# Optimization experiments

Hardware: AMD Instinct MI355X
Metric: run time of the kernel (lower is better)

Reference implementation:

```python
import jax, jax.numpy as jnp
import numpy as np

SIGMA = 5.67e-8  # Stefan-Boltzmann constant
NX = 13
N = NX * NX  # 169 nodes
B = 131072


def _build_matrices(L=0.1, thickness=0.001, board_k=15.0, emis=0.8):
    dx = L / (NX - 1)
    dy = L / (NX - 1)
    GLx = thickness * board_k * dy / dx
    GLy = thickness * board_k * dx / dy
    GR = 2.0 * dx * dy * emis
    iface = {0, NX - 1, NX * NX - 1, NX * NX - NX}
    K = np.zeros((N, N), dtype=np.float32)
    for j in range(NX):
        for i in range(NX):
            idn = i + NX * j
            if idn in iface:
                K[idn, idn] = 1.0
            else:
                gii = 0.0
                if i + 1 < NX:
                    K[idn, idn + 1] = -GLx  # east
                    gii += GLx
                if i - 1 >= 0:
                    K[idn, idn - 1] = -GLx  # west
                    gii += GLx
                if j + 1 < NX:
                    K[idn, idn + NX] = -GLx  # north (original code uses -GLx here too)
                    gii += GLy
                if j - 1 >= 0:
                    K[idn, idn - NX] = -GLx  # south (original code uses -GLx here too)
                    gii += GLy
                K[idn, idn] = gii
    e = np.full(N, GR, dtype=np.float32)
    for t in iface:
        e[t] = 0.0
    return jnp.asarray(K), jnp.asarray(e)


def setup_inputs() -> dict:
    key = jax.random.key(0)
    k1, k2, k3, k4 = jax.random.split(key, 4)
    # realistic temperatures (K) and heat loads (W)
    outputs = 270.0 + 60.0 * jax.random.uniform(k1, (B, NX, NX), dtype=jnp.float32)
    heaters = 0.5 * jax.random.uniform(k2, (B, NX, NX), dtype=jnp.float32)
    interfaces = 0.5 * jax.random.uniform(k3, (B, NX, NX), dtype=jnp.float32)
    Tenv = 270.0 + 30.0 * jax.random.uniform(k4, (B, 1), dtype=jnp.float32)
    K, e_diag = _build_matrices()
    return {"outputs": outputs, "heaters": heaters, "interfaces": interfaces,
            "Tenv": Tenv, "K": K, "e_diag": e_diag}


def reference(outputs, heaters, interfaces, Tenv, K, e_diag):
    b = outputs.shape[0]
    T = outputs.reshape(b, -1)                    # [B, 169]
    Q = heaters.reshape(b, -1) + interfaces.reshape(b, -1)  # [B, 169]
    # original computes K @ T_nodes_x_batch; batch-major equivalent is T @ K^T
    conduction = jnp.einsum('bn,mn->bm', T, K)    # [B, 169]
    radiation = SIGMA * e_diag[None, :] * (T ** 4 - Tenv ** 4)  # Tenv [B,1] broadcasts
    excess = conduction + radiation - Q
    return jnp.mean(jnp.abs(excess))
```

## Files before the change

### kernel.cpp

```cpp
#include <hip/hip_runtime.h>
#include <math.h>


#define SIGMA_F 5.67e-8f

constexpr int BLOCK = 256;

typedef float f4a __attribute__((ext_vector_type(4), aligned(4)));
typedef float f4b __attribute__((ext_vector_type(4), aligned(16)));

__global__ __launch_bounds__(256) void fused_residual_v7(
    const float* __restrict__ T,
    const float* __restrict__ H,
    const float* __restrict__ F,
    const float* __restrict__ Tenv,
    const float* __restrict__ K,
    const float* __restrict__ Ediag,
    float* __restrict__ partials,
    int total)
{
    __shared__ unsigned sTab[176];
    __shared__ float sred[BLOCK / 64];

    const float GLx = -K[1 * 169 + 2];
    const float GRs = SIGMA_F * Ediag[1];

    const int tid  = (int)threadIdx.x;
    const int lane = tid & 63;

    if (tid < 176) {
        int m = (tid < 169) ? tid : tid - 169;
        int ii = m % 13;
        unsigned cW = (ii > 0)   ? 1u : 0u;
        unsigned cE = (ii < 12)  ? 1u : 0u;
        unsigned cN = (m < 156)  ? 1u : 0u;
        unsigned cS = (m >= 13)  ? 1u : 0u;
        sTab[tid] = cW | (cE << 8) | (cN << 16) | (cS << 24);
    }
    __syncthreads();

    float acc = 0.0f;

    const int gstride = gridDim.x * BLOCK;
    for (int g = blockIdx.x * BLOCK + tid; g * 8 < total; g += gstride) {
        const int e0 = g * 8;
        const int waveBase = e0 - lane * 8;
        const bool fast = (waveBase >= 16) && (waveBase + 64 * 8 + 16 <= total);

        if (fast) {
            f4b t0 = *(const f4b*)(T + e0);
            f4b t1 = *(const f4b*)(T + e0 + 4);
            f4b h0 = __builtin_nontemporal_load((const f4b*)(H + e0));
            f4b h1 = __builtin_nontemporal_load((const f4b*)(H + e0 + 4));
            f4b f0 = __builtin_nontemporal_load((const f4b*)(F + e0));
            f4b f1 = __builtin_nontemporal_load((const f4b*)(F + e0 + 4));

            float sv[8];
            sv[0] = __shfl_up(t0.w, 2);
            sv[1] = __shfl_up(t1.x, 2);
            sv[2] = __shfl_up(t1.y, 2);
            sv[3] = __shfl_up(t1.z, 2);
            sv[4] = __shfl_up(t1.w, 2);
            sv[5] = __shfl_up(t0.x, 1);
            sv[6] = __shfl_up(t0.y, 1);
            sv[7] = __shfl_up(t0.z, 1);
            if (lane < 2) {
                f4a a = *(const f4a*)(T + e0 - 13);
                f4a b = *(const f4a*)(T + e0 - 9);
                sv[0] = a.x; sv[1] = a.y; sv[2] = a.z; sv[3] = a.w;
                sv[4] = b.x; sv[5] = b.y; sv[6] = b.z; sv[7] = b.w;
            }
            float nv[8];
            nv[0] = __shfl_down(t1.y, 1);
            nv[1] = __shfl_down(t1.z, 1);
            nv[2] = __shfl_down(t1.w, 1);
            nv[3] = __shfl_down(t0.x, 2);
            nv[4] = __shfl_down(t0.y, 2);
            nv[5] = __shfl_down(t0.z, 2);
            nv[6] = __shfl_down(t0.w, 2);
            nv[7] = __shfl_down(t1.x, 2);
            if (lane >= 62) {
                f4a a = *(const f4a*)(T + e0 + 13);
                f4a b = *(const f4a*)(T + e0 + 17);
                nv[0] = a.x; nv[1] = a.y; nv[2] = a.z; nv[3] = a.w;
                nv[4] = b.x; nv[5] = b.y; nv[6] = b.z; nv[7] = b.w;
            }
            float left = __shfl_up(t1.w, 1);
            if (lane == 0) left = T[e0 - 1];
            float right = __shfl_down(t0.x, 1);
            if (lane == 63) right = T[e0 + 8];

            const unsigned ue = (unsigned)e0;
            const unsigned b0 = ue / 169u;
            const int m0 = (int)(ue - b0 * 169u);

            float tvA = Tenv[b0];
            float tvB = tvA;
            if (m0 >= 162) tvB = Tenv[b0 + 1];
            const float tv4A = (tvA * tvA) * (tvA * tvA);
            const float tv4B = (tvB * tvB) * (tvB * tvB);

            const float tCv[8] = {t0.x, t0.y, t0.z, t0.w, t1.x, t1.y, t1.z, t1.w};
            const float tWv[8] = {left, t0.x, t0.y, t0.z, t0.w, t1.x, t1.y, t1.z};
            const float tEv[8] = {t0.y, t0.z, t0.w, t1.x, t1.y, t1.z, t1.w, right};
            const float hq[8]  = {h0.x + f0.x, h0.y + f0.y, h0.z + f0.z, h0.w + f0.w,
                                  h1.x + f1.x, h1.y + f1.y, h1.z + f1.z, h1.w + f1.w};

            #pragma unroll
            for (int j = 0; j < 8; ++j) {
                const unsigned w = sTab[m0 + j];
                const float mW = (float)(w & 0xffu);
                const float mE = (float)((w >> 8) & 0xffu);
                const float mN = (float)((w >> 16) & 0xffu);
                const float mS = (float)(w >> 24);

                const float t = tCv[j];
                float s = mW * tWv[j];
                s = fmaf(mE, tEv[j], s);
                s = fmaf(mN, nv[j], s);
                s = fmaf(mS, sv[j], s);
                const float nn = (mW + mE) + (mN + mS);
                const float q  = hq[j];
                const float tv4 = (m0 + j >= 169) ? tv4B : tv4A;
                const float t2 = t * t;
                const float d  = fmaf(t2, t2, -tv4);
                const float core = fmaf(GLx, fmaf(nn, t, -s), fmaf(GRs, d, -q));
                const float ex = (nn == 2.0f) ? (t - q) : core;
                acc += fabsf(ex);
            }
        } else {
            #pragma unroll
            for (int j = 0; j < 8; ++j) {
                int e = e0 + j;
                if (e >= total) break;
                unsigned b = (unsigned)e / 169u;
                int m = e - (int)b * 169;
                unsigned q13 = (unsigned)m / 13u;
                int ii = m - (int)q13 * 13;
                bool cE = (ii < 12), cW = (ii > 0), cN = (m < 156), cS = (m >= 13);
                bool ifc = (m == 0) | (m == 12) | (m == 156) | (m == 168);
                float t  = T[e];
                float tEv2 = cE ? T[e + 1]  : 0.0f;
                float tWv2 = cW ? T[e - 1]  : 0.0f;
                float tNv2 = cN ? T[e + 13] : 0.0f;
                float tSv2 = cS ? T[e - 13] : 0.0f;
                float s  = tEv2 + tWv2 + tNv2 + tSv2;
                float nn = (float)((int)cE + (int)cW + (int)cN + (int)cS);
                float tv = Tenv[b];
                float tv4 = (tv * tv) * (tv * tv);
                float t2 = t * t, t4 = t2 * t2;
                float qq = H[e] + F[e];
                float ex = ifc ? (t - qq)
                               : (GLx * (nn * t - s) + GRs * (t4 - tv4) - qq);
                acc += fabsf(ex);
            }
        }
    }

    #pragma unroll
    for (int off = 32; off > 0; off >>= 1)
        acc += __shfl_down(acc, off, 64);
    const int wid = tid >> 6;
    if (lane == 0) sred[wid] = acc;
    __syncthreads();
    if (tid == 0) {
        float s = 0.0f;
        #pragma unroll
        for (int w = 0; w < BLOCK / 64; ++w) s += sred[w];
        partials[blockIdx.x] = s;
    }
}

__global__ __launch_bounds__(256) void finalize_kernel(
    const float* __restrict__ partials, int n,
    float* __restrict__ out, float inv_total)
{
    __shared__ float sred[BLOCK / 64];
    float acc = 0.0f;
    for (int i = (int)threadIdx.x; i < n; i += BLOCK) acc += partials[i];
    #pragma unroll
    for (int off = 32; off > 0; off >>= 1)
        acc += __shfl_down(acc, off, 64);
    int lane = threadIdx.x & 63;
    int wid  = threadIdx.x >> 6;
    if (lane == 0) sred[wid] = acc;
    __syncthreads();
    if (threadIdx.x == 0) {
        float s = 0.0f;
        #pragma unroll
        for (int w = 0; w < BLOCK / 64; ++w) s += sred[w];
        out[0] = s * inv_total;
    }
}

extern "C" void kernel_launch(void* const* d_in, const int* in_sizes, int n_in,
                              void* d_out, int out_size, void* d_ws, size_t ws_size,
                              hipStream_t stream) {
    const float* T    = (const float*)d_in[0];
    const float* H    = (const float*)d_in[1];
    const float* F    = (const float*)d_in[2];
    const float* Tenv = (const float*)d_in[3];
    const float* K    = (const float*)d_in[4];
    const float* E    = (const float*)d_in[5];
    float* out      = (float*)d_out;
    float* partials = (float*)d_ws;

    const int total = in_sizes[0];

    int grid = (total / 8 + BLOCK - 1) / BLOCK;
    if ((size_t)grid * sizeof(float) > ws_size) grid = (int)(ws_size / sizeof(float));
    if (grid < 1) grid = 1;

    fused_residual_v7<<<grid, BLOCK, 0, stream>>>(T, H, F, Tenv, K, E, partials, total);

    const float inv_total = 1.0f / (float)total;
    finalize_kernel<<<1, BLOCK, 0, stream>>>(partials, grid, out, inv_total);
}
```

Before: 244.8 us.

## Software-pipeline loads in a persistent grid-stride loop with capped grid

Switches from one block per work tile to a fixed grid of 2048 blocks that loop grid-stride. Each iteration prefetches the next tile's T/H/F vectors into registers before computing the current one, with a sched_barrier to keep the loads issued early. The aim is to hide memory latency and cut block launch overhead. In exchange it raises register pressure, which may lower occupancy, and the sTab table grows to 184 entries.

Measured after the change: 243.2 us. About the same (-0.7%).

```diff
diff --git a/kernel.cpp b/kernel.cpp
--- a/kernel.cpp
+++ b/kernel.cpp
@@ -9,7 +9,7 @@
 typedef float f4a __attribute__((ext_vector_type(4), aligned(4)));
 typedef float f4b __attribute__((ext_vector_type(4), aligned(16)));
 
-__global__ __launch_bounds__(256) void fused_residual_v7(
+__global__ __launch_bounds__(256) void fused_residual_v10(
     const float* __restrict__ T,
     const float* __restrict__ H,
     const float* __restrict__ F,
@@ -19,7 +19,7 @@
     float* __restrict__ partials,
     int total)
 {
-    __shared__ unsigned sTab[176];
+    __shared__ unsigned sTab[184];
     __shared__ float sred[BLOCK / 64];
 
     const float GLx = -K[1 * 169 + 2];
@@ -28,13 +28,13 @@
     const int tid  = (int)threadIdx.x;
     const int lane = tid & 63;
 
-    if (tid < 176) {
+    if (tid < 184) {
         int m = (tid < 169) ? tid : tid - 169;
         int ii = m % 13;
-        unsigned cW = (ii > 0)   ? 1u : 0u;
-        unsigned cE = (ii < 12)  ? 1u : 0u;
-        unsigned cN = (m < 156)  ? 1u : 0u;
-        unsigned cS = (m >= 13)  ? 1u : 0u;
+        unsigned cW = (ii > 0)  ? 1u : 0u;
+        unsigned cE = (ii < 12) ? 1u : 0u;
+        unsigned cN = (m < 156) ? 1u : 0u;
+        unsigned cS = (m >= 13) ? 1u : 0u;
         sTab[tid] = cW | (cE << 8) | (cN << 16) | (cS << 24);
     }
     __syncthreads();
@@ -42,28 +42,56 @@
     float acc = 0.0f;
 
     const int gstride = gridDim.x * BLOCK;
-    for (int g = blockIdx.x * BLOCK + tid; g * 8 < total; g += gstride) {
+
+    auto isfast = [&](int gg) -> bool {
+        const int wb = gg * 8 - lane * 8;
+        return (wb >= 16) && (wb + 64 * 8 + 16 <= total);
+    };
+
+    int  g        = (int)blockIdx.x * BLOCK + tid;
+    bool haveCur  = (g * 8 < total);
+    bool fastCur  = haveCur && isfast(g);
+
+    f4b ct0, ct1, ch0, ch1, cf0, cf1;
+    if (fastCur) {
         const int e0 = g * 8;
-        const int waveBase = e0 - lane * 8;
-        const bool fast = (waveBase >= 16) && (waveBase + 64 * 8 + 16 <= total);
-
-        if (fast) {
-            f4b t0 = *(const f4b*)(T + e0);
-            f4b t1 = *(const f4b*)(T + e0 + 4);
-            f4b h0 = __builtin_nontemporal_load((const f4b*)(H + e0));
-            f4b h1 = __builtin_nontemporal_load((const f4b*)(H + e0 + 4));
-            f4b f0 = __builtin_nontemporal_load((const f4b*)(F + e0));
-            f4b f1 = __builtin_nontemporal_load((const f4b*)(F + e0 + 4));
+        ct0 = *(const f4b*)(T + e0);
+        ct1 = *(const f4b*)(T + e0 + 4);
+        ch0 = __builtin_nontemporal_load((const f4b*)(H + e0));
+        ch1 = __builtin_nontemporal_load((const f4b*)(H + e0 + 4));
+        cf0 = __builtin_nontemporal_load((const f4b*)(F + e0));
+        cf1 = __builtin_nontemporal_load((const f4b*)(F + e0 + 4));
+    }
+
+    while (haveCur) {
+        const int  gn    = g + gstride;
+        const bool haveN = (gn * 8 < total);
+        const bool fastN = haveN && isfast(gn);
+
+        f4b pt0, pt1, ph0, ph1, pf0, pf1;
+        if (fastN) {
+            const int en = gn * 8;
+            pt0 = *(const f4b*)(T + en);
+            pt1 = *(const f4b*)(T + en + 4);
+            ph0 = __builtin_nontemporal_load((const f4b*)(H + en));
+            ph1 = __builtin_nontemporal_load((const f4b*)(H + en + 4));
+            pf0 = __builtin_nontemporal_load((const f4b*)(F + en));
+            pf1 = __builtin_nontemporal_load((const f4b*)(F + en + 4));
+        }
+        __builtin_amdgcn_sched_barrier(0);
+
+        if (fastCur) {
+            const int e0 = g * 8;
 
             float sv[8];
-            sv[0] = __shfl_up(t0.w, 2);
-            sv[1] = __shfl_up(t1.x, 2);
-            sv[2] = __shfl_up(t1.y, 2);
-            sv[3] = __shfl_up(t1.z, 2);
-            sv[4] = __shfl_up(t1.w, 2);
-            sv[5] = __shfl_up(t0.x, 1);
-            sv[6] = __shfl_up(t0.y, 1);
-            sv[7] = __shfl_up(t0.z, 1);
+            sv[0] = __shfl_up(ct0.w, 2);
+            sv[1] = __shfl_up(ct1.x, 2);
+            sv[2] = __shfl_up(ct1.y, 2);
+            sv[3] = __shfl_up(ct1.z, 2);
+            sv[4] = __shfl_up(ct1.w, 2);
+            sv[5] = __shfl_up(ct0.x, 1);
+            sv[6] = __shfl_up(ct0.y, 1);
+            sv[7] = __shfl_up(ct0.z, 1);
             if (lane < 2) {
                 f4a a = *(const f4a*)(T + e0 - 13);
                 f4a b = *(const f4a*)(T + e0 - 9);
@@ -71,23 +99,23 @@
                 sv[4] = b.x; sv[5] = b.y; sv[6] = b.z; sv[7] = b.w;
             }
             float nv[8];
-            nv[0] = __shfl_down(t1.y, 1);
-            nv[1] = __shfl_down(t1.z, 1);
-            nv[2] = __shfl_down(t1.w, 1);
-            nv[3] = __shfl_down(t0.x, 2);
-            nv[4] = __shfl_down(t0.y, 2);
-            nv[5] = __shfl_down(t0.z, 2);
-            nv[6] = __shfl_down(t0.w, 2);
-            nv[7] = __shfl_down(t1.x, 2);
+            nv[0] = __shfl_down(ct1.y, 1);
+            nv[1] = __shfl_down(ct1.z, 1);
+            nv[2] = __shfl_down(ct1.w, 1);
+            nv[3] = __shfl_down(ct0.x, 2);
+            nv[4] = __shfl_down(ct0.y, 2);
+            nv[5] = __shfl_down(ct0.z, 2);
+            nv[6] = __shfl_down(ct0.w, 2);
+            nv[7] = __shfl_down(ct1.x, 2);
             if (lane >= 62) {
                 f4a a = *(const f4a*)(T + e0 + 13);
                 f4a b = *(const f4a*)(T + e0 + 17);
                 nv[0] = a.x; nv[1] = a.y; nv[2] = a.z; nv[3] = a.w;
                 nv[4] = b.x; nv[5] = b.y; nv[6] = b.z; nv[7] = b.w;
             }
-            float left = __shfl_up(t1.w, 1);
+            float left = __shfl_up(ct1.w, 1);
             if (lane == 0) left = T[e0 - 1];
-            float right = __shfl_down(t0.x, 1);
+            float right = __shfl_down(ct0.x, 1);
             if (lane == 63) right = T[e0 + 8];
 
             const unsigned ue = (unsigned)e0;
@@ -100,11 +128,16 @@
             const float tv4A = (tvA * tvA) * (tvA * tvA);
             const float tv4B = (tvB * tvB) * (tvB * tvB);
 
-            const float tCv[8] = {t0.x, t0.y, t0.z, t0.w, t1.x, t1.y, t1.z, t1.w};
-            const float tWv[8] = {left, t0.x, t0.y, t0.z, t0.w, t1.x, t1.y, t1.z};
-            const float tEv[8] = {t0.y, t0.z, t0.w, t1.x, t1.y, t1.z, t1.w, right};
-            const float hq[8]  = {h0.x + f0.x, h0.y + f0.y, h0.z + f0.z, h0.w + f0.w,
-                                  h1.x + f1.x, h1.y + f1.y, h1.z + f1.z, h1.w + f1.w};
+            const float tCv[8] = {ct0.x, ct0.y, ct0.z, ct0.w,
+                                  ct1.x, ct1.y, ct1.z, ct1.w};
+            const float tWv[8] = {left, ct0.x, ct0.y, ct0.z,
+                                  ct0.w, ct1.x, ct1.y, ct1.z};
+            const float tEv[8] = {ct0.y, ct0.z, ct0.w, ct1.x,
+                                  ct1.y, ct1.z, ct1.w, right};
+            const float hq[8]  = {ch0.x + cf0.x, ch0.y + cf0.y,
+                                  ch0.z + cf0.z, ch0.w + cf0.w,
+                                  ch1.x + cf1.x, ch1.y + cf1.y,
+                                  ch1.z + cf1.z, ch1.w + cf1.w};
 
             #pragma unroll
             for (int j = 0; j < 8; ++j) {
@@ -129,6 +162,7 @@
                 acc += fabsf(ex);
             }
         } else {
+            const int e0 = g * 8;
             #pragma unroll
             for (int j = 0; j < 8; ++j) {
                 int e = e0 + j;
@@ -155,6 +189,11 @@
                 acc += fabsf(ex);
             }
         }
+
+        ct0 = pt0; ct1 = pt1; ch0 = ph0; ch1 = ph1; cf0 = pf0; cf1 = pf1;
+        fastCur = fastN;
+        haveCur = haveN;
+        g = gn;
     }
 
     #pragma unroll
@@ -207,11 +246,14 @@
 
     const int total = in_sizes[0];
 
-    int grid = (total / 8 + BLOCK - 1) / BLOCK;
+    int grid = 2048;
+    const int work = (total / 8 + BLOCK - 1) / BLOCK;
+    if (grid > work) grid = work > 0 ? work : 1;
     if ((size_t)grid * sizeof(float) > ws_size) grid = (int)(ws_size / sizeof(float));
     if (grid < 1) grid = 1;
 
-    fused_residual_v7<<<grid, BLOCK, 0, stream>>>(T, H, F, Tenv, K, E, partials, total);
+    fused_residual_v10<<<grid, BLOCK, 0, stream>>>(T, H, F, Tenv, K, E, partials,
+                                                   total);
 
     const float inv_total = 1.0f / (float)total;
     finalize_kernel<<<1, BLOCK, 0, stream>>>(partials, grid, out, inv_total);
```

## Double-buffer grid-stride loads with a persistent fixed-size grid

Applied to the files above, without the earlier changes.

Replaces the one-shot-per-thread grid with a persistent grid of 1352 blocks that loops over the data grid-stride. Each step prefetches the next chunk's T/H/F loads into a second register buffer while the current chunk is computed, with sched_barrier keeping the loads ahead of the compute. The goal is to hide memory latency and cut block launch overhead. In exchange it uses more registers, which may lower occupancy, and the slow path issues dummy loads at offset 16.

Measured after the change: 252.5 us. 3.1% more time.

```diff
diff --git a/kernel.cpp b/kernel.cpp
--- a/kernel.cpp
+++ b/kernel.cpp
@@ -9,7 +9,145 @@
 typedef float f4a __attribute__((ext_vector_type(4), aligned(4)));
 typedef float f4b __attribute__((ext_vector_type(4), aligned(16)));
 
-__global__ __launch_bounds__(256) void fused_residual_v7(
+struct Buf { f4b t0, t1, h0, h1, f0, f1; };
+
+static __device__ __forceinline__ void loadbuf(
+    Buf& b, const float* __restrict__ T, const float* __restrict__ H,
+    const float* __restrict__ F, int e0, bool fast)
+{
+    const int e = fast ? e0 : 16;
+    b.t0 = *(const f4b*)(T + e);
+    b.t1 = *(const f4b*)(T + e + 4);
+    b.h0 = __builtin_nontemporal_load((const f4b*)(H + e));
+    b.h1 = __builtin_nontemporal_load((const f4b*)(H + e + 4));
+    b.f0 = __builtin_nontemporal_load((const f4b*)(F + e));
+    b.f1 = __builtin_nontemporal_load((const f4b*)(F + e + 4));
+}
+
+static __device__ __forceinline__ float compute_fast(
+    const Buf& b, int e0, int lane,
+    const float* __restrict__ T, const float* __restrict__ Tenv,
+    const unsigned* sTab, float GLx, float GRs)
+{
+    float acc = 0.0f;
+
+    float sv[8];
+    sv[0] = __shfl_up(b.t0.w, 2);
+    sv[1] = __shfl_up(b.t1.x, 2);
+    sv[2] = __shfl_up(b.t1.y, 2);
+    sv[3] = __shfl_up(b.t1.z, 2);
+    sv[4] = __shfl_up(b.t1.w, 2);
+    sv[5] = __shfl_up(b.t0.x, 1);
+    sv[6] = __shfl_up(b.t0.y, 1);
+    sv[7] = __shfl_up(b.t0.z, 1);
+    if (lane < 2) {
+        f4a a = *(const f4a*)(T + e0 - 13);
+        f4a c = *(const f4a*)(T + e0 - 9);
+        sv[0] = a.x; sv[1] = a.y; sv[2] = a.z; sv[3] = a.w;
+        sv[4] = c.x; sv[5] = c.y; sv[6] = c.z; sv[7] = c.w;
+    }
+    float nv[8];
+    nv[0] = __shfl_down(b.t1.y, 1);
+    nv[1] = __shfl_down(b.t1.z, 1);
+    nv[2] = __shfl_down(b.t1.w, 1);
+    nv[3] = __shfl_down(b.t0.x, 2);
+    nv[4] = __shfl_down(b.t0.y, 2);
+    nv[5] = __shfl_down(b.t0.z, 2);
+    nv[6] = __shfl_down(b.t0.w, 2);
+    nv[7] = __shfl_down(b.t1.x, 2);
+    if (lane >= 62) {
+        f4a a = *(const f4a*)(T + e0 + 13);
+        f4a c = *(const f4a*)(T + e0 + 17);
+        nv[0] = a.x; nv[1] = a.y; nv[2] = a.z; nv[3] = a.w;
+        nv[4] = c.x; nv[5] = c.y; nv[6] = c.z; nv[7] = c.w;
+    }
+    float left = __shfl_up(b.t1.w, 1);
+    if (lane == 0) left = T[e0 - 1];
+    float right = __shfl_down(b.t0.x, 1);
+    if (lane == 63) right = T[e0 + 8];
+
+    const unsigned ue = (unsigned)e0;
+    const unsigned b0 = ue / 169u;
+    const int m0 = (int)(ue - b0 * 169u);
+
+    float tvA = Tenv[b0];
+    float tvB = tvA;
+    if (m0 >= 162) tvB = Tenv[b0 + 1];
+    const float tv4A = (tvA * tvA) * (tvA * tvA);
+    const float tv4B = (tvB * tvB) * (tvB * tvB);
+
+    const float tCv[8] = {b.t0.x, b.t0.y, b.t0.z, b.t0.w,
+                          b.t1.x, b.t1.y, b.t1.z, b.t1.w};
+    const float tWv[8] = {left, b.t0.x, b.t0.y, b.t0.z,
+                          b.t0.w, b.t1.x, b.t1.y, b.t1.z};
+    const float tEv[8] = {b.t0.y, b.t0.z, b.t0.w, b.t1.x,
+                          b.t1.y, b.t1.z, b.t1.w, right};
+    const float hq[8]  = {b.h0.x + b.f0.x, b.h0.y + b.f0.y,
+                          b.h0.z + b.f0.z, b.h0.w + b.f0.w,
+                          b.h1.x + b.f1.x, b.h1.y + b.f1.y,
+                          b.h1.z + b.f1.z, b.h1.w + b.f1.w};
+
+    #pragma unroll
+    for (int j = 0; j < 8; ++j) {
+        const unsigned w = sTab[m0 + j];
+        const float mW = (float)(w & 0xffu);
+        const float mE = (float)((w >> 8) & 0xffu);
+        const float mN = (float)((w >> 16) & 0xffu);
+        const float mS = (float)(w >> 24);
+
+        const float t = tCv[j];
+        float s = mW * tWv[j];
+        s = fmaf(mE, tEv[j], s);
+        s = fmaf(mN, nv[j], s);
+        s = fmaf(mS, sv[j], s);
+        const float nn = (mW + mE) + (mN + mS);
+        const float q  = hq[j];
+        const float tv4 = (m0 + j >= 169) ? tv4B : tv4A;
+        const float t2 = t * t;
+        const float d  = fmaf(t2, t2, -tv4);
+        const float core = fmaf(GLx, fmaf(nn, t, -s), fmaf(GRs, d, -q));
+        const float ex = (nn == 2.0f) ? (t - q) : core;
+        acc += fabsf(ex);
+    }
+    return acc;
+}
+
+static __device__ __forceinline__ float compute_slow(
+    int e0, int total,
+    const float* __restrict__ T, const float* __restrict__ H,
+    const float* __restrict__ F, const float* __restrict__ Tenv,
+    float GLx, float GRs)
+{
+    float acc = 0.0f;
+    #pragma unroll
+    for (int j = 0; j < 8; ++j) {
+        int e = e0 + j;
+        if (e >= total) break;
+        unsigned bb = (unsigned)e / 169u;
+        int m = e - (int)bb * 169;
+        unsigned q13 = (unsigned)m / 13u;
+        int ii = m - (int)q13 * 13;
+        bool cE = (ii < 12), cW = (ii > 0), cN = (m < 156), cS = (m >= 13);
+        bool ifc = (m == 0) | (m == 12) | (m == 156) | (m == 168);
+        float t  = T[e];
+        float tEv = cE ? T[e + 1]  : 0.0f;
+        float tWv = cW ? T[e - 1]  : 0.0f;
+        float tNv = cN ? T[e + 13] : 0.0f;
+        float tSv = cS ? T[e - 13] : 0.0f;
+        float s  = tEv + tWv + tNv + tSv;
+        float nn = (float)((int)cE + (int)cW + (int)cN + (int)cS);
+        float tv = Tenv[bb];
+        float tv4 = (tv * tv) * (tv * tv);
+        float t2 = t * t, t4 = t2 * t2;
+        float qq = H[e] + F[e];
+        float ex = ifc ? (t - qq)
+                       : (GLx * (nn * t - s) + GRs * (t4 - tv4) - qq);
+        acc += fabsf(ex);
+    }
+    return acc;
+}
+
+__global__ __launch_bounds__(256) void fused_residual_v11(
     const float* __restrict__ T,
     const float* __restrict__ H,
     const float* __restrict__ F,
@@ -19,7 +157,7 @@
     float* __restrict__ partials,
     int total)
 {
-    __shared__ unsigned sTab[176];
+    __shared__ unsigned sTab[184];
     __shared__ float sred[BLOCK / 64];
 
     const float GLx = -K[1 * 169 + 2];
@@ -28,133 +166,58 @@
     const int tid  = (int)threadIdx.x;
     const int lane = tid & 63;
 
-    if (tid < 176) {
+    if (tid < 184) {
         int m = (tid < 169) ? tid : tid - 169;
         int ii = m % 13;
-        unsigned cW = (ii > 0)   ? 1u : 0u;
-        unsigned cE = (ii < 12)  ? 1u : 0u;
-        unsigned cN = (m < 156)  ? 1u : 0u;
-        unsigned cS = (m >= 13)  ? 1u : 0u;
+        unsigned cW = (ii > 0)  ? 1u : 0u;
+        unsigned cE = (ii < 12) ? 1u : 0u;
+        unsigned cN = (m < 156) ? 1u : 0u;
+        unsigned cS = (m >= 13) ? 1u : 0u;
         sTab[tid] = cW | (cE << 8) | (cN << 16) | (cS << 24);
     }
     __syncthreads();
 
     float acc = 0.0f;
 
-    const int gstride = gridDim.x * BLOCK;
-    for (int g = blockIdx.x * BLOCK + tid; g * 8 < total; g += gstride) {
-        const int e0 = g * 8;
-        const int waveBase = e0 - lane * 8;
-        const bool fast = (waveBase >= 16) && (waveBase + 64 * 8 + 16 <= total);
-
-        if (fast) {
-            f4b t0 = *(const f4b*)(T + e0);
-            f4b t1 = *(const f4b*)(T + e0 + 4);
-            f4b h0 = __builtin_nontemporal_load((const f4b*)(H + e0));
-            f4b h1 = __builtin_nontemporal_load((const f4b*)(H + e0 + 4));
-            f4b f0 = __builtin_nontemporal_load((const f4b*)(F + e0));
-            f4b f1 = __builtin_nontemporal_load((const f4b*)(F + e0 + 4));
-
-            float sv[8];
-            sv[0] = __shfl_up(t0.w, 2);
-            sv[1] = __shfl_up(t1.x, 2);
-            sv[2] = __shfl_up(t1.y, 2);
-            sv[3] = __shfl_up(t1.z, 2);
-            sv[4] = __shfl_up(t1.w, 2);
-            sv[5] = __shfl_up(t0.x, 1);
-            sv[6] = __shfl_up(t0.y, 1);
-            sv[7] = __shfl_up(t0.z, 1);
-            if (lane < 2) {
-                f4a a = *(const f4a*)(T + e0 - 13);
-                f4a b = *(const f4a*)(T + e0 - 9);
-                sv[0] = a.x; sv[1] = a.y; sv[2] = a.z; sv[3] = a.w;
-                sv[4] = b.x; sv[5] = b.y; sv[6] = b.z; sv[7] = b.w;
-            }
-            float nv[8];
-            nv[0] = __shfl_down(t1.y, 1);
-            nv[1] = __shfl_down(t1.z, 1);
-            nv[2] = __shfl_down(t1.w, 1);
-            nv[3] = __shfl_down(t0.x, 2);
-            nv[4] = __shfl_down(t0.y, 2);
-            nv[5] = __shfl_down(t0.z, 2);
-            nv[6] = __shfl_down(t0.w, 2);
-            nv[7] = __shfl_down(t1.x, 2);
-            if (lane >= 62) {
-                f4a a = *(const f4a*)(T + e0 + 13);
-                f4a b = *(const f4a*)(T + e0 + 17);
-                nv[0] = a.x; nv[1] = a.y; nv[2] = a.z; nv[3] = a.w;
-                nv[4] = b.x; nv[5] = b.y; nv[6] = b.z; nv[7] = b.w;
-            }
-            float left = __shfl_up(t1.w, 1);
-            if (lane == 0) left = T[e0 - 1];
-            float right = __shfl_down(t0.x, 1);
-            if (lane == 63) right = T[e0 + 8];
-
-            const unsigned ue = (unsigned)e0;
-            const unsigned b0 = ue / 169u;
-            const int m0 = (int)(ue - b0 * 169u);
-
-            float tvA = Tenv[b0];
-            float tvB = tvA;
-            if (m0 >= 162) tvB = Tenv[b0 + 1];
-            const float tv4A = (tvA * tvA) * (tvA * tvA);
-            const float tv4B = (tvB * tvB) * (tvB * tvB);
-
-            const float tCv[8] = {t0.x, t0.y, t0.z, t0.w, t1.x, t1.y, t1.z, t1.w};
-            const float tWv[8] = {left, t0.x, t0.y, t0.z, t0.w, t1.x, t1.y, t1.z};
-            const float tEv[8] = {t0.y, t0.z, t0.w, t1.x, t1.y, t1.z, t1.w, right};
-            const float hq[8]  = {h0.x + f0.x, h0.y + f0.y, h0.z + f0.z, h0.w + f0.w,
-                                  h1.x + f1.x, h1.y + f1.y, h1.z + f1.z, h1.w + f1.w};
-
-            #pragma unroll
-            for (int j = 0; j < 8; ++j) {
-                const unsigned w = sTab[m0 + j];
-                const float mW = (float)(w & 0xffu);
-                const float mE = (float)((w >> 8) & 0xffu);
-                const float mN = (float)((w >> 16) & 0xffu);
-                const float mS = (float)(w >> 24);
-
-                const float t = tCv[j];
-                float s = mW * tWv[j];
-                s = fmaf(mE, tEv[j], s);
-                s = fmaf(mN, nv[j], s);
-                s = fmaf(mS, sv[j], s);
-                const float nn = (mW + mE) + (mN + mS);
-                const float q  = hq[j];
-                const float tv4 = (m0 + j >= 169) ? tv4B : tv4A;
-                const float t2 = t * t;
-                const float d  = fmaf(t2, t2, -tv4);
-                const float core = fmaf(GLx, fmaf(nn, t, -s), fmaf(GRs, d, -q));
-                const float ex = (nn == 2.0f) ? (t - q) : core;
-                acc += fabsf(ex);
-            }
-        } else {
-            #pragma unroll
-            for (int j = 0; j < 8; ++j) {
-                int e = e0 + j;
-                if (e >= total) break;
-                unsigned b = (unsigned)e / 169u;
-                int m = e - (int)b * 169;
-                unsigned q13 = (unsigned)m / 13u;
-                int ii = m - (int)q13 * 13;
-                bool cE = (ii < 12), cW = (ii > 0), cN = (m < 156), cS = (m >= 13);
-                bool ifc = (m == 0) | (m == 12) | (m == 156) | (m == 168);
-                float t  = T[e];
-                float tEv2 = cE ? T[e + 1]  : 0.0f;
-                float tWv2 = cW ? T[e - 1]  : 0.0f;
-                float tNv2 = cN ? T[e + 13] : 0.0f;
-                float tSv2 = cS ? T[e - 13] : 0.0f;
-                float s  = tEv2 + tWv2 + tNv2 + tSv2;
-                float nn = (float)((int)cE + (int)cW + (int)cN + (int)cS);
-                float tv = Tenv[b];
-                float tv4 = (tv * tv) * (tv * tv);
-                float t2 = t * t, t4 = t2 * t2;
-                float qq = H[e] + F[e];
-                float ex = ifc ? (t - qq)
-                               : (GLx * (nn * t - s) + GRs * (t4 - tv4) - qq);
-                acc += fabsf(ex);
-            }
-        }
+    const int stride = (int)gridDim.x * BLOCK;
+
+    auto isfast = [&](int gg) -> bool {
+        const int wb = gg * 8 - lane * 8;
+        return (wb >= 16) && (wb + 64 * 8 + 16 <= total);
+    };
+
+    int  gA = (int)blockIdx.x * BLOCK + tid;
+    bool vA = (gA * 8 < total);
+    bool fA = vA && isfast(gA);
+
+    Buf A, B;
+    loadbuf(A, T, H, F, gA * 8, fA);
+    __builtin_amdgcn_sched_barrier(0);
+
+    while (vA) {
+        const int  gB = gA + stride;
+        const bool vB = (gB * 8 < total);
+        const bool fB = vB && isfast(gB);
+
+        loadbuf(B, T, H, F, gB * 8, fB);
+        __builtin_amdgcn_sched_barrier(0);
+
+        if (fA) acc += compute_fast(A, gA * 8, lane, T, Tenv, sTab, GLx, GRs);
+        else    acc += compute_slow(gA * 8, total, T, H, F, Tenv, GLx, GRs);
+
+        if (!vB) break;
+
+        const int  gA2 = gB + stride;
+        const bool vA2 = (gA2 * 8 < total);
+        const bool fA2 = vA2 && isfast(gA2);
+
+        loadbuf(A, T, H, F, gA2 * 8, fA2);
+        __builtin_amdgcn_sched_barrier(0);
+
+        if (fB) acc += compute_fast(B, gB * 8, lane, T, Tenv, sTab, GLx, GRs);
+        else    acc += compute_slow(gB * 8, total, T, H, F, Tenv, GLx, GRs);
+
+        gA = gA2; vA = vA2; fA = fA2;
     }
 
     #pragma unroll
@@ -207,11 +270,14 @@
 
     const int total = in_sizes[0];
 
-    int grid = (total / 8 + BLOCK - 1) / BLOCK;
+    int grid = 1352;
+    const int work = (total / 8 + BLOCK - 1) / BLOCK;
+    if (grid > work) grid = work > 0 ? work : 1;
     if ((size_t)grid * sizeof(float) > ws_size) grid = (int)(ws_size / sizeof(float));
     if (grid < 1) grid = 1;
 
-    fused_residual_v7<<<grid, BLOCK, 0, stream>>>(T, H, F, Tenv, K, E, partials, total);
+    fused_residual_v11<<<grid, BLOCK, 0, stream>>>(T, H, F, Tenv, K, E, partials,
+                                                   total);
 
     const float inv_total = 1.0f / (float)total;
     finalize_kernel<<<1, BLOCK, 0, stream>>>(partials, grid, out, inv_total);
```
